# Kernel tuning notes

Hardware: AMD Instinct MI355X
Metric: run time of the kernel (lower is better)

Reference implementation:

```python
import math
import jax, jax.numpy as jnp
import numpy as np

# config (matches env defaults of the torch module, scaled to production size)
V, D, L, NH, NKV, MLP_M, RECUR, N_VB = 32768, 1024, 6, 16, 8, 3, 2, 5
BG_BK, BG_DIM = 4096, 128
HD = D // NH            # 64 head dim
KV = NKV * HD           # 512 kv width
B, T = 2, 1024
SOFTCAP = 30.0
EPS = 1.1920929e-07     # fp32 eps used by F.rms_norm(eps=None)


def _rms(x):
    return x * jax.lax.rsqrt(jnp.mean(jnp.square(x), axis=-1, keepdims=True) + EPS)


def _rope(x, c, s):
    h = x.shape[-1] // 2
    x1, x2 = x[..., :h], x[..., h:]
    return jnp.concatenate([x1 * c + x2 * s, -x1 * s + x2 * c], axis=-1)


def _forward(ids, tgt, emb, bg_embed, bg_proj, bg_scale, ve,
             Wq, Wk, Wv, Wo, qg, a_s, m_s, mix, Wfc, Wpr):
    Bz, Tz = ids.shape
    # token embedding + bigram-hash embedding
    x = emb[ids]
    t = ids.astype(jnp.int32)
    hv = jnp.bitwise_xor(t[:, 1:] * 36313, t[:, :-1] * 27191) % (BG_BK - 1)
    h = jnp.zeros_like(t).at[:, 1:].set(hv)
    bg = (bg_embed[h] @ bg_proj) * bg_scale
    x = _rms(x + bg)
    x0 = x
    # rope tables
    inv = 1.0 / (10000.0 ** (jnp.arange(0, HD, 2, dtype=jnp.float32) / HD))
    ang = jnp.arange(Tz, dtype=jnp.float32)[:, None] * inv      # (T, HD/2)
    c, s = jnp.cos(ang)[None, None], jnp.sin(ang)[None, None]   # (1,1,T,HD/2)
    mask = jnp.tril(jnp.ones((Tz, Tz), dtype=bool))
    eff = 0
    for _ in range(RECUR):
        for l in range(L):
            vel = ve[eff % N_VB][ids]                            # (B,T,KV)
            m = mix[l]
            x = m[0] * x + m[1] * x0
            # attention
            xn = _rms(x)
            q = (xn @ Wq[l]).reshape(Bz, Tz, NH, HD).transpose(0, 2, 1, 3)
            k = (xn @ Wk[l]).reshape(Bz, Tz, NKV, HD).transpose(0, 2, 1, 3)
            v = ((xn @ Wv[l]) + vel).reshape(Bz, Tz, NKV, HD).transpose(0, 2, 1, 3)
            q, k = _rms(q), _rms(k)
            q, k = _rope(q, c, s), _rope(k, c, s)
            q = q * qg[l][None, :, None, None]
            rep = NH // NKV                                      # GQA expand
            kf = jnp.repeat(k, rep, axis=1)
            vf = jnp.repeat(v, rep, axis=1)
            sc = jnp.einsum('bhqd,bhkd->bhqk', q, kf) / math.sqrt(HD)
            sc = jnp.where(mask, sc, -jnp.inf)
            att = jax.nn.softmax(sc, axis=-1)
            y = jnp.einsum('bhqk,bhkd->bhqd', att, vf)
            y = y.transpose(0, 2, 1, 3).reshape(Bz, Tz, D) @ Wo[l]
            x = x + a_s[l] * y
            # mlp: relu(fc(x))^2 @ proj
            hmid = jnp.square(jax.nn.relu(_rms(x) @ Wfc[l]))
            x = x + m_s[l] * (hmid @ Wpr[l])
            eff += 1
    x = _rms(x)
    lo = x @ emb.T
    lo = SOFTCAP * jnp.tanh(lo / SOFTCAP)
    logp = jax.nn.log_softmax(lo, axis=-1)
    nll = -jnp.take_along_axis(logp, tgt[..., None], axis=-1)[..., 0]
    return jnp.mean(nll)


def setup_inputs() -> dict:
    key = jax.random.key(0)
    ks = jax.random.split(key, 14)
    def nrm(k, shape, std):
        return std * jax.random.normal(k, shape, dtype=jnp.float32)
    eff = L * RECUR
    return {
        'ids': jax.random.randint(ks[0], (B, T), 0, V),
        'tgt': jax.random.randint(ks[1], (B, T), 0, V),
        'emb': nrm(ks[2], (V, D), 0.005),
        'bg_embed': nrm(ks[3], (BG_BK, BG_DIM), 0.02),
        'bg_proj': nrm(ks[4], (BG_DIM, D), 1.0 / math.sqrt(BG_DIM)),
        'bg_scale': jnp.float32(0.05),
        've': nrm(ks[5], (N_VB, V, KV), 0.01),
        'Wq': nrm(ks[6], (L, D, D), 1.0 / math.sqrt(D)),
        'Wk': nrm(ks[7], (L, D, KV), 1.0 / math.sqrt(D)),
        'Wv': nrm(ks[8], (L, D, KV), 1.0 / math.sqrt(D)),
        'Wo': nrm(ks[9], (L, D, D), 1.0 / (math.sqrt(D) * math.sqrt(2 * eff))),
        'qg': jnp.full((L, NH), 1.5, jnp.float32),
        'a_s': jnp.ones((L, D), jnp.float32),
        'm_s': jnp.ones((L, D), jnp.float32),
        'mix': jnp.stack([jnp.ones((L, D)), jnp.zeros((L, D))], axis=1).astype(jnp.float32),
        'Wfc': nrm(ks[10], (L, D, MLP_M * D), 1.0 / math.sqrt(D)),
        'Wpr': nrm(ks[11], (L, MLP_M * D, D), 1.0 / (math.sqrt(MLP_M * D) * math.sqrt(2 * eff))),
    }


def reference(ids, tgt, emb, bg_embed, bg_proj, bg_scale, ve,
              Wq, Wk, Wv, Wo, qg, a_s, m_s, mix, Wfc, Wpr):
    return _forward(ids, tgt, emb, bg_embed, bg_proj, bg_scale, ve,
                    Wq, Wk, Wv, Wo, qg, a_s, m_s, mix, Wfc, Wpr)
```

## Files before the change

### kernel.cpp

```cpp
#include <hip/hip_runtime.h>
#include <hip/hip_bf16.h>
#include <math.h>

#define DEV __device__ __forceinline__

typedef unsigned short u16;
typedef short bf16x8 __attribute__((ext_vector_type(8)));
typedef float f32x4 __attribute__((ext_vector_type(4)));
typedef u16 u16x8 __attribute__((ext_vector_type(8)));
typedef u16 u16x4 __attribute__((ext_vector_type(4)));

#define T_SEQ 1024
#define NTOK 2048
#define DIM 1024
#define NHD 16
#define NKVH 8
#define HDIM 64
#define KVD 512
#define MLPD 3072
#define VOC 32768
#define EPSF 1.1920929e-07f
#define SCAP 30.0f
#define NCB 512

#define MEMFENCE asm volatile("" ::: "memory")

DEV u16 f2b(float f) {
  __hip_bfloat16 h = __float2bfloat16(f);
  u16 r; __builtin_memcpy(&r, &h, 2); return r;
}
DEV float b2f(u16 u) {
  __hip_bfloat16 h; __builtin_memcpy(&h, &u, 2);
  return __bfloat162float(h);
}

DEV void gload16(const void* g, void* l) {
  __builtin_amdgcn_global_load_lds((const __attribute__((address_space(1))) void*)g,
                                   (__attribute__((address_space(3))) void*)l, 16, 0, 0);
}

DEV float blk_sum256(float v, float* sbuf) {
#pragma unroll
  for (int o = 32; o; o >>= 1) v += __shfl_xor(v, o, 64);
  int w = threadIdx.x >> 6;
  if ((threadIdx.x & 63) == 0) sbuf[w] = v;
  __syncthreads();
  return sbuf[0] + sbuf[1] + sbuf[2] + sbuf[3];
}

__global__ __launch_bounds__(256) void transpose_f2b(const float* __restrict__ in,
    u16* __restrict__ out, int K, int N, size_t in_ls, size_t out_ls) {
  __shared__ float tile[32][33];
  int l = blockIdx.z;
  const float* src = in + (size_t)l * in_ls;
  u16* dst = out + (size_t)l * out_ls;
  int k0 = blockIdx.y << 5, n0 = blockIdx.x << 5;
  int tx = threadIdx.x & 31, ty = threadIdx.x >> 5;
#pragma unroll
  for (int i = 0; i < 32; i += 8)
    tile[ty + i][tx] = src[(size_t)(k0 + ty + i) * N + n0 + tx];
  __syncthreads();
#pragma unroll
  for (int i = 0; i < 32; i += 8)
    dst[(size_t)(n0 + ty + i) * K + k0 + tx] = f2b(tile[tx][ty + i]);
}

__global__ __launch_bounds__(256) void f2b_copy(const float* __restrict__ in,
    u16* __restrict__ out, size_t n) {
  size_t i = ((size_t)blockIdx.x * 256 + threadIdx.x) * 8;
  if (i >= n) return;
  float4 a = *(const float4*)(in + i);
  float4 b = *(const float4*)(in + i + 4);
  u16x8 o;
  o[0] = f2b(a.x); o[1] = f2b(a.y); o[2] = f2b(a.z); o[3] = f2b(a.w);
  o[4] = f2b(b.x); o[5] = f2b(b.y); o[6] = f2b(b.z); o[7] = f2b(b.w);
  *(u16x8*)(out + i) = o;
}

__global__ __launch_bounds__(256) void rope_table(float* __restrict__ rc, float* __restrict__ rs) {
  int idx = blockIdx.x * 256 + threadIdx.x;
  if (idx >= T_SEQ * 32) return;
  int t = idx >> 5, i = idx & 31;
  float inv = expf(-((float)(2 * i) / (float)HDIM) * logf(10000.0f));
  float ang = (float)t * inv;
  rc[idx] = cosf(ang);
  rs[idx] = sinf(ang);
}

__global__ __launch_bounds__(256) void embed_kernel(const int* __restrict__ ids,
    const float* __restrict__ emb, const float* __restrict__ bg_embed,
    const float* __restrict__ bg_proj, const float* __restrict__ bg_scale_p,
    float* __restrict__ x, float* __restrict__ x0) {
  __shared__ float be[128];
  __shared__ float sbuf[4];
  int tok = blockIdx.x, tid = threadIdx.x;
  int t = tok & (T_SEQ - 1);
  int id = ids[tok];
  int hsh = 0;
  if (t > 0) {
    int prev = ids[tok - 1];
    hsh = ((id * 36313) ^ (prev * 27191)) % 4095;
  }
  if (tid < 128) be[tid] = bg_embed[hsh * 128 + tid];
  __syncthreads();
  float scale = bg_scale_p[0];
  const float4* bp = (const float4*)bg_proj;
  float ax = 0.f, ay = 0.f, az = 0.f, aw = 0.f;
#pragma unroll 4
  for (int j = 0; j < 128; ++j) {
    float bj = be[j];
    float4 p = bp[j * 256 + tid];
    ax += bj * p.x; ay += bj * p.y; az += bj * p.z; aw += bj * p.w;
  }
  float4 e = *(const float4*)(emb + (size_t)id * DIM + tid * 4);
  float vx = e.x + ax * scale, vy = e.y + ay * scale;
  float vz = e.z + az * scale, vw = e.w + aw * scale;
  float ss = vx * vx + vy * vy + vz * vz + vw * vw;
  float tot = blk_sum256(ss, sbuf);
  float rn = rsqrtf(tot * (1.0f / DIM) + EPSF);
  float4 o; o.x = vx * rn; o.y = vy * rn; o.z = vz * rn; o.w = vw * rn;
  size_t base = (size_t)tok * DIM + tid * 4;
  *(float4*)(x + base) = o;
  *(float4*)(x0 + base) = o;
}

__global__ __launch_bounds__(256) void mix_rms(float* __restrict__ x,
    const float* __restrict__ x0, const float* __restrict__ mixl, u16* __restrict__ xn) {
  __shared__ float sbuf[4];
  int tok = blockIdx.x, tid = threadIdx.x;
  size_t base = (size_t)tok * DIM + tid * 4;
  float4 a = *(const float4*)(x + base);
  float4 b = *(const float4*)(x0 + base);
  float4 m0 = *(const float4*)(mixl + tid * 4);
  float4 m1 = *(const float4*)(mixl + DIM + tid * 4);
  float rx = m0.x * a.x + m1.x * b.x;
  float ry = m0.y * a.y + m1.y * b.y;
  float rz = m0.z * a.z + m1.z * b.z;
  float rw = m0.w * a.w + m1.w * b.w;
  float ss = rx * rx + ry * ry + rz * rz + rw * rw;
  float tot = blk_sum256(ss, sbuf);
  float rn = rsqrtf(tot * (1.0f / DIM) + EPSF);
  float4 o; o.x = rx; o.y = ry; o.z = rz; o.w = rw;
  *(float4*)(x + base) = o;
  u16x4 q;
  q[0] = f2b(rx * rn); q[1] = f2b(ry * rn); q[2] = f2b(rz * rn); q[3] = f2b(rw * rn);
  *(u16x4*)(xn + base) = q;
}

__global__ __launch_bounds__(256) void rms_only(const float* __restrict__ x, u16* __restrict__ out) {
  __shared__ float sbuf[4];
  int tok = blockIdx.x, tid = threadIdx.x;
  size_t base = (size_t)tok * DIM + tid * 4;
  float4 a = *(const float4*)(x + base);
  float ss = a.x * a.x + a.y * a.y + a.z * a.z + a.w * a.w;
  float tot = blk_sum256(ss, sbuf);
  float rn = rsqrtf(tot * (1.0f / DIM) + EPSF);
  u16x4 q;
  q[0] = f2b(a.x * rn); q[1] = f2b(a.y * rn); q[2] = f2b(a.z * rn); q[3] = f2b(a.w * rn);
  *(u16x4*)(out + base) = q;
}

template <int EPI, int BN>
__global__ __launch_bounds__(256, (BN == 64 ? 3 : 2)) void gemm_bt(
    const u16* __restrict__ A, const u16* __restrict__ Bt,
    float* __restrict__ Cf, u16* __restrict__ Cb, const float* __restrict__ colscale,
    int N, int K, int kpn) {
  constexpr int MF = (BN == 128) ? 4 : 2;
  constexpr int ASZ = 128 * 64;
  constexpr int BSZ = BN * 64;
  constexpr int NLD = 4 + BN / 32;
  __shared__ u16 As[2 * ASZ];
  __shared__ u16 Bs[2 * BSZ];
  int tid = threadIdx.x;
  int wid = tid >> 6, lane = tid & 63;
  int g = lane >> 4, c = lane & 15;
  int row0 = blockIdx.y << 7, col0 = blockIdx.x * BN;
  int kbase = blockIdx.z * kpn;
  int wr = (BN == 128) ? ((wid >> 1) << 6) : (wid << 5);
  int wc = (BN == 128) ? ((wid & 1) << 6) : 0;
  f32x4 acc[MF][4] = {};

  int sr = lane >> 3;
  int kb = lane & 7;
  const u16* srcA[4];
  int ldsA[4];
#pragma unroll
  for (int i = 0; i < 4; ++i) {
    int s = (wid << 2) + i;
    int r = (s << 3) + sr;
    srcA[i] = A + (size_t)(row0 + r) * K + kbase + ((kb ^ (r & 7)) << 3);
    ldsA[i] = s << 9;
  }
  const u16* srcB[BN / 32];
  int ldsB[BN / 32];
#pragma unroll
  for (int i = 0; i < BN / 32; ++i) {
    int s = wid * (BN / 32) + i;
    int r = (s << 3) + sr;
    srcB[i] = Bt + (size_t)(col0 + r) * K + kbase + ((kb ^ (r & 7)) << 3);
    ldsB[i] = s << 9;
  }

#pragma unroll
  for (int i = 0; i < 4; ++i) gload16(srcA[i], As + ldsA[i]);
#pragma unroll
  for (int i = 0; i < BN / 32; ++i) gload16(srcB[i], Bs + ldsB[i]);

  int nk = kpn >> 6;
  for (int t = 0; t < nk; ++t) {
    int cur = t & 1;
    if (t + 1 < nk) {
      int nxt = cur ^ 1;
      int ko = (t + 1) << 6;
#pragma unroll
      for (int i = 0; i < 4; ++i) gload16(srcA[i] + ko, As + nxt * ASZ + ldsA[i]);
#pragma unroll
      for (int i = 0; i < BN / 32; ++i) gload16(srcB[i] + ko, Bs + nxt * BSZ + ldsB[i]);
      if constexpr (NLD == 6) asm volatile("s_waitcnt vmcnt(6)" ::: "memory");
      else asm volatile("s_waitcnt vmcnt(8)" ::: "memory");
    } else {
      asm volatile("s_waitcnt vmcnt(0)" ::: "memory");
    }
    __builtin_amdgcn_s_barrier();
    MEMFENCE;
    const u16* ab = As + cur * ASZ;
    const u16* bb = Bs + cur * BSZ;
#pragma unroll
    for (int ks = 0; ks < 2; ++ks) {
      bf16x8 af[MF], bfr[4];
#pragma unroll
      for (int m = 0; m < MF; ++m) {
        int r = wr + m * 16 + c;
        int kbs = ((ks << 2) + g) ^ (r & 7);
        af[m] = *(const bf16x8*)(ab + r * 64 + (kbs << 3));
      }
#pragma unroll
      for (int n = 0; n < 4; ++n) {
        int r = wc + n * 16 + c;
        int kbs = ((ks << 2) + g) ^ (r & 7);
        bfr[n] = *(const bf16x8*)(bb + r * 64 + (kbs << 3));
      }
      __builtin_amdgcn_s_setprio(1);
#pragma unroll
      for (int m = 0; m < MF; ++m)
#pragma unroll
        for (int n = 0; n < 4; ++n)
          acc[m][n] = __builtin_amdgcn_mfma_f32_16x16x32_bf16(af[m], bfr[n], acc[m][n], 0, 0, 0);
      __builtin_amdgcn_s_setprio(0);
    }
    MEMFENCE;
    __builtin_amdgcn_s_barrier();
  }

#pragma unroll
  for (int m = 0; m < MF; ++m) {
#pragma unroll
    for (int n = 0; n < 4; ++n) {
      int gcol = col0 + wc + n * 16 + c;
#pragma unroll
      for (int j = 0; j < 4; ++j) {
        int grow = row0 + wr + m * 16 + g * 4 + j;
        float v = acc[m][n][j];
        if (EPI == 1) {
          atomicAdd(&Cf[(size_t)grow * N + gcol], colscale[gcol] * v);
        } else if (EPI == 2) {
          float r = v > 0.f ? v : 0.f;
          Cb[(size_t)grow * N + gcol] = f2b(r * r);
        }
      }
    }
  }
}

__global__ __launch_bounds__(512, 2) void gemm_lmhead(
    const u16* __restrict__ A, const u16* __restrict__ Bt,
    const int* __restrict__ tgt, float* __restrict__ pM, float* __restrict__ pS,
    float* __restrict__ loTgt) {
  constexpr int K = 1024;
  constexpr int TSZ = 256 * 64;
  __shared__ u16 As[2 * TSZ];
  __shared__ u16 Bs[2 * TSZ];
  int tid = threadIdx.x;
  int wid = tid >> 6, lane = tid & 63;
  int wm = wid >> 2, wn = wid & 3;
  int g = lane >> 4, c = lane & 15;
  int row0 = blockIdx.y << 8, col0 = blockIdx.x << 8;
  f32x4 acc[8][4] = {};

  int sr = lane >> 3, kb = lane & 7;
  const u16* srcA[4];
  const u16* srcB[4];
  int ldsOff[4];
#pragma unroll
  for (int i = 0; i < 4; ++i) {
    int s = (wid << 2) + i;
    int r = (s << 3) + sr;
    srcA[i] = A + (size_t)(row0 + r) * K + ((kb ^ (r & 7)) << 3);
    srcB[i] = Bt + (size_t)(col0 + r) * K + ((kb ^ (r & 7)) << 3);
    ldsOff[i] = s << 9;
  }

#pragma unroll
  for (int i = 0; i < 4; ++i) {
    gload16(srcA[i], As + ldsOff[i]);
    gload16(srcB[i], Bs + ldsOff[i]);
  }

  constexpr int nk = K >> 6;
  for (int kt = 0; kt < nk; ++kt) {
    int cur = kt & 1;
    if (kt + 1 < nk) {
      int nxt = cur ^ 1;
      int ko = (kt + 1) << 6;
#pragma unroll
      for (int i = 0; i < 4; ++i) {
        gload16(srcA[i] + ko, As + nxt * TSZ + ldsOff[i]);
        gload16(srcB[i] + ko, Bs + nxt * TSZ + ldsOff[i]);
      }
      asm volatile("s_waitcnt vmcnt(8)" ::: "memory");
    } else {
      asm volatile("s_waitcnt vmcnt(0)" ::: "memory");
    }
    __builtin_amdgcn_s_barrier();
    MEMFENCE;
    const u16* ab = As + cur * TSZ;
    const u16* bb = Bs + cur * TSZ;
    bf16x8 bfr[4][2];
#pragma unroll
    for (int nf = 0; nf < 4; ++nf) {
      int r = (wn << 6) + nf * 16 + c;
#pragma unroll
      for (int ks = 0; ks < 2; ++ks) {
        int kbs = ((ks << 2) + g) ^ (r & 7);
        bfr[nf][ks] = *(const bf16x8*)(bb + r * 64 + (kbs << 3));
      }
    }
#pragma unroll
    for (int p = 0; p < 4; ++p) {
      bf16x8 af[2][2];
#pragma unroll
      for (int mi = 0; mi < 2; ++mi) {
        int r = (wm << 7) + ((p << 1) + mi) * 16 + c;
#pragma unroll
        for (int ks = 0; ks < 2; ++ks) {
          int kbs = ((ks << 2) + g) ^ (r & 7);
          af[mi][ks] = *(const bf16x8*)(ab + r * 64 + (kbs << 3));
        }
      }
      __builtin_amdgcn_s_setprio(1);
#pragma unroll
      for (int ks = 0; ks < 2; ++ks)
#pragma unroll
        for (int mi = 0; mi < 2; ++mi)
#pragma unroll
          for (int nf = 0; nf < 4; ++nf)
            acc[(p << 1) + mi][nf] = __builtin_amdgcn_mfma_f32_16x16x32_bf16(
                af[mi][ks], bfr[nf][ks], acc[(p << 1) + mi][nf], 0, 0, 0);
      __builtin_amdgcn_s_setprio(0);
    }
    MEMFENCE;
    __builtin_amdgcn_s_barrier();
  }

  int cb = (col0 >> 6) + wn;
#pragma unroll
  for (int mf = 0; mf < 8; ++mf) {
#pragma unroll
    for (int j = 0; j < 4; ++j) {
      int grow = row0 + (wm << 7) + mf * 16 + g * 4 + j;
      int tg = tgt[grow];
      float sv[4];
      float mx = -3.0e38f;
#pragma unroll
      for (int nf = 0; nf < 4; ++nf) {
        float a = acc[mf][nf][j] * (1.0f / SCAP);
        a = fminf(fmaxf(a, -15.f), 15.f);
        float e = __expf(2.0f * a);
        float tt = SCAP * (e - 1.0f) / (e + 1.0f);
        sv[nf] = tt;
        mx = fmaxf(mx, tt);
        int gcol = col0 + (wn << 6) + nf * 16 + c;
        if (gcol == tg) loTgt[grow] = tt;
      }
      mx = fmaxf(mx, __shfl_xor(mx, 1, 64));
      mx = fmaxf(mx, __shfl_xor(mx, 2, 64));
      mx = fmaxf(mx, __shfl_xor(mx, 4, 64));
      mx = fmaxf(mx, __shfl_xor(mx, 8, 64));
      float s = 0.f;
#pragma unroll
      for (int nf = 0; nf < 4; ++nf) s += __expf(sv[nf] - mx);
      s += __shfl_xor(s, 1, 64);
      s += __shfl_xor(s, 2, 64);
      s += __shfl_xor(s, 4, 64);
      s += __shfl_xor(s, 8, 64);
      if (c == 0) {
        pM[(size_t)grow * NCB + cb] = mx;
        pS[(size_t)grow * NCB + cb] = s;
      }
    }
  }
}

__global__ __launch_bounds__(256, 3) void gemm_qkv(
    const u16* __restrict__ A, const u16* __restrict__ Bt,
    const float* __restrict__ qg_l, const float* __restrict__ rc, const float* __restrict__ rs,
    const float* __restrict__ ve, const int* __restrict__ ids, int vb,
    u16* __restrict__ qB, u16* __restrict__ kB, u16* __restrict__ vT) {
  constexpr int K = 1024;
  constexpr int ASZ = 128 * 64;
  constexpr int BSZ = 64 * 64;
  __shared__ u16 As[2 * ASZ];
  __shared__ u16 Bs[2 * BSZ];
  int tid = threadIdx.x;
  int wid = tid >> 6, lane = tid & 63;
  int g = lane >> 4, c = lane & 15;
  int bx = blockIdx.x;
  int row0 = blockIdx.y << 7, col0 = bx << 6;
  f32x4 acc[2][4] = {};

  int sr = lane >> 3, kb = lane & 7;
  const u16* srcA[4];
  int ldsA[4];
#pragma unroll
  for (int i = 0; i < 4; ++i) {
    int s = (wid << 2) + i;
    int r = (s << 3) + sr;
    srcA[i] = A + (size_t)(row0 + r) * K + ((kb ^ (r & 7)) << 3);
    ldsA[i] = s << 9;
  }
  const u16* srcB[2];
  int ldsB[2];
#pragma unroll
  for (int i = 0; i < 2; ++i) {
    int s = (wid << 1) + i;
    int r = (s << 3) + sr;
    srcB[i] = Bt + (size_t)(col0 + r) * K + ((kb ^ (r & 7)) << 3);
    ldsB[i] = s << 9;
  }

#pragma unroll
  for (int i = 0; i < 4; ++i) gload16(srcA[i], As + ldsA[i]);
#pragma unroll
  for (int i = 0; i < 2; ++i) gload16(srcB[i], Bs + ldsB[i]);

  for (int t = 0; t < 16; ++t) {
    int cur = t & 1;
    if (t + 1 < 16) {
      int nxt = cur ^ 1;
      int ko = (t + 1) << 6;
#pragma unroll
      for (int i = 0; i < 4; ++i) gload16(srcA[i] + ko, As + nxt * ASZ + ldsA[i]);
#pragma unroll
      for (int i = 0; i < 2; ++i) gload16(srcB[i] + ko, Bs + nxt * BSZ + ldsB[i]);
      asm volatile("s_waitcnt vmcnt(6)" ::: "memory");
    } else {
      asm volatile("s_waitcnt vmcnt(0)" ::: "memory");
    }
    __builtin_amdgcn_s_barrier();
    MEMFENCE;
    const u16* ab = As + cur * ASZ;
    const u16* bb = Bs + cur * BSZ;
#pragma unroll
    for (int ks = 0; ks < 2; ++ks) {
      bf16x8 af[2], bfr[4];
#pragma unroll
      for (int m = 0; m < 2; ++m) {
        int r = (wid << 5) + m * 16 + c;
        int kbs = ((ks << 2) + g) ^ (r & 7);
        af[m] = *(const bf16x8*)(ab + r * 64 + (kbs << 3));
      }
#pragma unroll
      for (int n = 0; n < 4; ++n) {
        int r = n * 16 + c;
        int kbs = ((ks << 2) + g) ^ (r & 7);
        bfr[n] = *(const bf16x8*)(bb + r * 64 + (kbs << 3));
      }
      __builtin_amdgcn_s_setprio(1);
#pragma unroll
      for (int m = 0; m < 2; ++m)
#pragma unroll
        for (int n = 0; n < 4; ++n)
          acc[m][n] = __builtin_amdgcn_mfma_f32_16x16x32_bf16(af[m], bfr[n], acc[m][n], 0, 0, 0);
      __builtin_amdgcn_s_setprio(0);
    }
    MEMFENCE;
    __builtin_amdgcn_s_barrier();
  }

  int b = row0 >> 10;
  if (bx < 24) {
    bool isq = (bx < 16);
    int h = isq ? bx : bx - 16;
    float gmul = isq ? qg_l[h] * 0.125f : 1.0f;
    u16* hb = isq ? (qB + ((size_t)(b * NHD + h)) * T_SEQ * HDIM)
                  : (kB + ((size_t)(b * NKVH + h)) * T_SEQ * HDIM);
#pragma unroll
    for (int m = 0; m < 2; ++m) {
#pragma unroll
      for (int j = 0; j < 4; ++j) {
        int grow = row0 + (wid << 5) + m * 16 + g * 4 + j;
        int t = grow & (T_SEQ - 1);
        float vv[4];
        float ss = 0.f;
#pragma unroll
        for (int n = 0; n < 4; ++n) { vv[n] = acc[m][n][j]; ss += vv[n] * vv[n]; }
        ss += __shfl_xor(ss, 1, 64);
        ss += __shfl_xor(ss, 2, 64);
        ss += __shfl_xor(ss, 4, 64);
        ss += __shfl_xor(ss, 8, 64);
        float rn = rsqrtf(ss * (1.0f / HDIM) + EPSF);
#pragma unroll
        for (int n = 0; n < 4; ++n) vv[n] *= rn;
        float c0 = rc[t * 32 + c], s0 = rs[t * 32 + c];
        float c1 = rc[t * 32 + 16 + c], s1 = rs[t * 32 + 16 + c];
        float o0 = vv[0] * c0 + vv[2] * s0;
        float o1 = vv[1] * c1 + vv[3] * s1;
        float o2 = vv[2] * c0 - vv[0] * s0;
        float o3 = vv[3] * c1 - vv[1] * s1;
        u16* dst = hb + (size_t)t * HDIM;
        dst[c] = f2b(o0 * gmul);
        dst[16 + c] = f2b(o1 * gmul);
        dst[32 + c] = f2b(o2 * gmul);
        dst[48 + c] = f2b(o3 * gmul);
      }
    }
  } else {
    int kh = bx - 24;
#pragma unroll
    for (int m = 0; m < 2; ++m) {
#pragma unroll
      for (int j = 0; j < 4; ++j) {
        int grow = row0 + (wid << 5) + m * 16 + g * 4 + j;
        int lr = (wid << 5) + m * 16 + g * 4 + j;
        int id = ids[grow];
        const float* vl = ve + ((size_t)vb * VOC + id) * KVD + kh * HDIM;
#pragma unroll
        for (int n = 0; n < 4; ++n)
          As[lr * 72 + n * 16 + c] = f2b(acc[m][n][j] + vl[n * 16 + c]);
      }
    }
    __syncthreads();
    int hd = tid & 63, seg = tid >> 6;
    int t0 = (row0 & (T_SEQ - 1)) + seg * 32;
    u16* dst = vT + (((size_t)(b * NKVH + kh)) * HDIM + hd) * T_SEQ + t0;
#pragma unroll
    for (int i = 0; i < 32; i += 8) {
      u16x8 o;
#pragma unroll
      for (int e = 0; e < 8; ++e) o[e] = As[(seg * 32 + i + e) * 72 + hd];
      *(u16x8*)(dst + i) = o;
    }
  }
}

__global__ __launch_bounds__(128) void attn_kernel(const u16* __restrict__ qB,
    const u16* __restrict__ kB, const u16* __restrict__ vT, const float* __restrict__ qg_l,
    u16* __restrict__ attout) {
  __shared__ u16 plds[2][32 * 76];
  int b = blockIdx.z, h = blockIdx.y;
  int kh = h >> 1;
  int wid = threadIdx.x >> 6, lane = threadIdx.x & 63;
  int g = lane >> 4, c = lane & 15;
  int strip = wid ? (31 - (int)blockIdx.x) : (int)blockIdx.x;
  int qr0 = strip << 5;
  const u16* qptr = qB + ((size_t)(b * NHD + h)) * T_SEQ * HDIM;
  const u16* kptr = kB + ((size_t)(b * NKVH + kh)) * T_SEQ * HDIM;
  const u16* vptr = vT + ((size_t)(b * NKVH + kh)) * HDIM * T_SEQ;
  u16* pw = plds[wid];
  float Mh = fabsf(qg_l[h]) * 8.0f;

  bf16x8 aq[2][2];
#pragma unroll
  for (int m = 0; m < 2; ++m)
#pragma unroll
    for (int ks = 0; ks < 2; ++ks)
      aq[m][ks] = *(const bf16x8*)(qptr + (qr0 + m * 16 + c) * HDIM + ks * 32 + g * 8);

  bf16x8 vone;
#pragma unroll
  for (int e = 0; e < 8; ++e) vone[e] = (short)0x3F80;

  f32x4 oacc[2][4] = {};
  f32x4 lacc[2] = {};

  for (int kv0 = 0; kv0 <= qr0; kv0 += 64) {
    bf16x8 bk[4][2];
#pragma unroll
    for (int n = 0; n < 4; ++n)
#pragma unroll
      for (int ks = 0; ks < 2; ++ks)
        bk[n][ks] = *(const bf16x8*)(kptr + (kv0 + n * 16 + c) * HDIM + ks * 32 + g * 8);
    f32x4 sc[2][4] = {};
#pragma unroll
    for (int ks = 0; ks < 2; ++ks)
#pragma unroll
      for (int m = 0; m < 2; ++m)
#pragma unroll
        for (int n = 0; n < 4; ++n)
          sc[m][n] = __builtin_amdgcn_mfma_f32_16x16x32_bf16(aq[m][ks], bk[n][ks], sc[m][n], 0, 0, 0);
    bool maskT = (kv0 + 64 > qr0);
#pragma unroll
    for (int m = 0; m < 2; ++m) {
#pragma unroll
      for (int j = 0; j < 4; ++j) {
        int row = qr0 + m * 16 + g * 4 + j;
        float p0 = __expf(sc[m][0][j] - Mh);
        float p1 = __expf(sc[m][1][j] - Mh);
        float p2 = __expf(sc[m][2][j] - Mh);
        float p3 = __expf(sc[m][3][j] - Mh);
        if (maskT) {
          if (kv0 + c > row) p0 = 0.f;
          if (kv0 + 16 + c > row) p1 = 0.f;
          if (kv0 + 32 + c > row) p2 = 0.f;
          if (kv0 + 48 + c > row) p3 = 0.f;
        }
        int pr = m * 16 + g * 4 + j;
        pw[pr * 76 + c] = f2b(p0);
        pw[pr * 76 + 16 + c] = f2b(p1);
        pw[pr * 76 + 32 + c] = f2b(p2);
        pw[pr * 76 + 48 + c] = f2b(p3);
      }
    }
    MEMFENCE;
    bf16x8 ap[2][2];
#pragma unroll
    for (int m = 0; m < 2; ++m)
#pragma unroll
      for (int ks = 0; ks < 2; ++ks) {
        u16x8 tmp = *(const u16x8*)(pw + (m * 16 + c) * 76 + ks * 32 + g * 8);
        __builtin_memcpy(&ap[m][ks], &tmp, 16);
      }
    bf16x8 bv[4][2];
#pragma unroll
    for (int n = 0; n < 4; ++n)
#pragma unroll
      for (int ks = 0; ks < 2; ++ks)
        bv[n][ks] = *(const bf16x8*)(vptr + (n * 16 + c) * T_SEQ + kv0 + ks * 32 + g * 8);
#pragma unroll
    for (int ks = 0; ks < 2; ++ks) {
#pragma unroll
      for (int m = 0; m < 2; ++m) {
#pragma unroll
        for (int n = 0; n < 4; ++n)
          oacc[m][n] = __builtin_amdgcn_mfma_f32_16x16x32_bf16(ap[m][ks], bv[n][ks], oacc[m][n], 0, 0, 0);
        lacc[m] = __builtin_amdgcn_mfma_f32_16x16x32_bf16(ap[m][ks], vone, lacc[m], 0, 0, 0);
      }
    }
  }

#pragma unroll
  for (int m = 0; m < 2; ++m) {
#pragma unroll
    for (int j = 0; j < 4; ++j) {
      float inv = 1.0f / lacc[m][j];
      int trow = qr0 + m * 16 + g * 4 + j;
      u16* orow = attout + ((size_t)(b * T_SEQ + trow)) * DIM + h * HDIM;
#pragma unroll
      for (int n = 0; n < 4; ++n)
        orow[n * 16 + c] = f2b(oacc[m][n][j] * inv);
    }
  }
}

__global__ __launch_bounds__(256) void lse_merge(const float* __restrict__ pM,
    const float* __restrict__ pS, const float* __restrict__ loTgt, float* __restrict__ nll) {
  __shared__ float sbuf[4];
  int tok = blockIdx.x, tid = threadIdx.x;
  int wid = tid >> 6, lane = tid & 63;
  const float* rm = pM + (size_t)tok * NCB;
  const float* rs = pS + (size_t)tok * NCB;
  float m0 = rm[tid], m1 = rm[tid + 256];
  float mx = fmaxf(m0, m1);
#pragma unroll
  for (int o = 32; o; o >>= 1) mx = fmaxf(mx, __shfl_xor(mx, o, 64));
  if (lane == 0) sbuf[wid] = mx;
  __syncthreads();
  float M = fmaxf(fmaxf(sbuf[0], sbuf[1]), fmaxf(sbuf[2], sbuf[3]));
  __syncthreads();
  float s = rs[tid] * __expf(m0 - M) + rs[tid + 256] * __expf(m1 - M);
  float S = blk_sum256(s, sbuf);
  if (tid == 0) nll[tok] = logf(S) + M - loTgt[tok];
}

__global__ __launch_bounds__(256) void loss_final(const float* __restrict__ nll,
    float* __restrict__ out) {
  __shared__ float sbuf[4];
  int tid = threadIdx.x;
  float acc = 0.f;
  for (int i = tid; i < NTOK; i += 256) acc += nll[i];
  float tot = blk_sum256(acc, sbuf);
  if (tid == 0) out[0] = tot * (1.0f / NTOK);
}

extern "C" void kernel_launch(void* const* d_in, const int* in_sizes, int n_in,
                              void* d_out, int out_size, void* d_ws, size_t ws_size,
                              hipStream_t stream) {
  (void)in_sizes; (void)n_in; (void)out_size; (void)ws_size;
  const int* ids = (const int*)d_in[0];
  const int* tgt = (const int*)d_in[1];
  const float* emb = (const float*)d_in[2];
  const float* bg_embed = (const float*)d_in[3];
  const float* bg_proj = (const float*)d_in[4];
  const float* bg_scale = (const float*)d_in[5];
  const float* ve = (const float*)d_in[6];
  const float* Wq = (const float*)d_in[7];
  const float* Wk = (const float*)d_in[8];
  const float* Wv = (const float*)d_in[9];
  const float* Wo = (const float*)d_in[10];
  const float* qg = (const float*)d_in[11];
  const float* a_s = (const float*)d_in[12];
  const float* m_s = (const float*)d_in[13];
  const float* mix = (const float*)d_in[14];
  const float* Wfc = (const float*)d_in[15];
  const float* Wpr = (const float*)d_in[16];

  char* w = (char*)d_ws;
  auto alloc = [&](size_t bytes) {
    char* p = w;
    w += (bytes + 255) & ~(size_t)255;
    return p;
  };
  u16* WqkvT = (u16*)alloc(6ull * 2048 * 1024 * 2);
  u16* WoT   = (u16*)alloc(6ull * 1024 * 1024 * 2);
  u16* WfcT  = (u16*)alloc(6ull * 3072 * 1024 * 2);
  u16* WprT  = (u16*)alloc(6ull * 1024 * 3072 * 2);
  u16* embB  = (u16*)alloc((size_t)VOC * DIM * 2);
  float* x   = (float*)alloc((size_t)NTOK * DIM * 4);
  float* x0  = (float*)alloc((size_t)NTOK * DIM * 4);
  u16* xn    = (u16*)alloc((size_t)NTOK * DIM * 2);
  u16* qBuf  = (u16*)alloc((size_t)NTOK * DIM * 2);
  u16* kBuf  = (u16*)alloc((size_t)NTOK * KVD * 2);
  u16* vTb   = (u16*)alloc((size_t)NTOK * KVD * 2);
  u16* attout = (u16*)alloc((size_t)NTOK * DIM * 2);
  u16* xmlp  = (u16*)alloc((size_t)NTOK * DIM * 2);
  u16* hmid  = (u16*)alloc((size_t)NTOK * MLPD * 2);
  float* rc  = (float*)alloc((size_t)T_SEQ * 32 * 4);
  float* rs  = (float*)alloc((size_t)T_SEQ * 32 * 4);
  float* pM  = (float*)alloc((size_t)NTOK * NCB * 4);
  float* pS  = (float*)alloc((size_t)NTOK * NCB * 4);
  float* loTgt = (float*)alloc(NTOK * 4);
  float* nll = (float*)alloc(NTOK * 4);

  transpose_f2b<<<dim3(32, 32, 6), 256, 0, stream>>>(Wq, WqkvT, 1024, 1024,
      (size_t)1024 * 1024, (size_t)2048 * 1024);
  transpose_f2b<<<dim3(16, 32, 6), 256, 0, stream>>>(Wk, WqkvT + 1024 * 1024, 1024, 512,
      (size_t)1024 * 512, (size_t)2048 * 1024);
  transpose_f2b<<<dim3(16, 32, 6), 256, 0, stream>>>(Wv, WqkvT + 1536 * 1024, 1024, 512,
      (size_t)1024 * 512, (size_t)2048 * 1024);
  transpose_f2b<<<dim3(32, 32, 6), 256, 0, stream>>>(Wo, WoT, 1024, 1024,
      (size_t)1024 * 1024, (size_t)1024 * 1024);
  transpose_f2b<<<dim3(96, 32, 6), 256, 0, stream>>>(Wfc, WfcT, 1024, 3072,
      (size_t)1024 * 3072, (size_t)3072 * 1024);
  transpose_f2b<<<dim3(32, 96, 6), 256, 0, stream>>>(Wpr, WprT, 3072, 1024,
      (size_t)3072 * 1024, (size_t)1024 * 3072);
  f2b_copy<<<16384, 256, 0, stream>>>(emb, embB, (size_t)VOC * DIM);
  rope_table<<<128, 256, 0, stream>>>(rc, rs);
  embed_kernel<<<NTOK, 256, 0, stream>>>(ids, emb, bg_embed, bg_proj, bg_scale, x, x0);

  for (int step = 0; step < 12; ++step) {
    int l = step % 6;
    mix_rms<<<NTOK, 256, 0, stream>>>(x, x0, mix + l * 2048, xn);
    gemm_qkv<<<dim3(32, 16), 256, 0, stream>>>(xn, WqkvT + (size_t)l * 2048 * 1024,
        qg + l * 16, rc, rs, ve, ids, step % 5, qBuf, kBuf, vTb);
    attn_kernel<<<dim3(16, 16, 2), 128, 0, stream>>>(qBuf, kBuf, vTb, qg + l * 16, attout);
    gemm_bt<1, 64><<<dim3(16, 16, 2), 256, 0, stream>>>(attout, WoT + (size_t)l * 1024 * 1024,
        x, nullptr, a_s + l * DIM, 1024, 1024, 512);
    rms_only<<<NTOK, 256, 0, stream>>>(x, xmlp);
    gemm_bt<2, 128><<<dim3(24, 16, 1), 256, 0, stream>>>(xmlp, WfcT + (size_t)l * 3072 * 1024,
        nullptr, hmid, nullptr, 3072, 1024, 1024);
    gemm_bt<1, 64><<<dim3(16, 16, 3), 256, 0, stream>>>(hmid, WprT + (size_t)l * 1024 * 3072,
        x, nullptr, m_s + l * DIM, 1024, 3072, 1024);
  }

  rms_only<<<NTOK, 256, 0, stream>>>(x, xn);
  gemm_lmhead<<<dim3(128, 8), 512, 0, stream>>>(xn, embB, tgt, pM, pS, loTgt);
  lse_merge<<<NTOK, 256, 0, stream>>>(pM, pS, loTgt, nll);
  loss_final<<<1, 256, 0, stream>>>(nll, (float*)d_out);
}
```

Baseline: 2.089 ms.

## Replace split-K atomic accumulation with partial buffers reduced in norm kernels

The split-K output-projection and MLP-projection GEMMs now write plain stores into per-split partial buffers instead of doing float atomicAdd into the residual. The following norm kernel sums the partials, applies the per-column scale, updates the residual and computes the RMS norm, which merges mix_rms and rms_only into one templated kernel. The LM-head GEMM also gets a 1D grid with a block-index swizzle so blocks sharing the same weight columns run close together, for better L2 reuse. The cost is a 24MB partial buffer and more memory traffic in the norm kernels.

```diff
diff --git a/kernel.cpp b/kernel.cpp
--- a/kernel.cpp
+++ b/kernel.cpp
@@ -22,6 +22,7 @@
 #define EPSF 1.1920929e-07f
 #define SCAP 30.0f
 #define NCB 512
+#define PSTRIDE ((size_t)NTOK * DIM)
 
 #define MEMFENCE asm volatile("" ::: "memory")
 
@@ -124,46 +125,50 @@
   *(float4*)(x0 + base) = o;
 }
 
-__global__ __launch_bounds__(256) void mix_rms(float* __restrict__ x,
-    const float* __restrict__ x0, const float* __restrict__ mixl, u16* __restrict__ xn) {
+template <int NP, int MIX>
+__global__ __launch_bounds__(256) void norm_k(float* __restrict__ x,
+    const float* __restrict__ parts, const float* __restrict__ colscale,
+    const float* __restrict__ mixl, const float* __restrict__ x0,
+    u16* __restrict__ xn) {
   __shared__ float sbuf[4];
   int tok = blockIdx.x, tid = threadIdx.x;
   size_t base = (size_t)tok * DIM + tid * 4;
   float4 a = *(const float4*)(x + base);
-  float4 b = *(const float4*)(x0 + base);
-  float4 m0 = *(const float4*)(mixl + tid * 4);
-  float4 m1 = *(const float4*)(mixl + DIM + tid * 4);
-  float rx = m0.x * a.x + m1.x * b.x;
-  float ry = m0.y * a.y + m1.y * b.y;
-  float rz = m0.z * a.z + m1.z * b.z;
-  float rw = m0.w * a.w + m1.w * b.w;
-  float ss = rx * rx + ry * ry + rz * rz + rw * rw;
-  float tot = blk_sum256(ss, sbuf);
-  float rn = rsqrtf(tot * (1.0f / DIM) + EPSF);
-  float4 o; o.x = rx; o.y = ry; o.z = rz; o.w = rw;
-  *(float4*)(x + base) = o;
-  u16x4 q;
-  q[0] = f2b(rx * rn); q[1] = f2b(ry * rn); q[2] = f2b(rz * rn); q[3] = f2b(rw * rn);
-  *(u16x4*)(xn + base) = q;
-}
-
-__global__ __launch_bounds__(256) void rms_only(const float* __restrict__ x, u16* __restrict__ out) {
-  __shared__ float sbuf[4];
-  int tok = blockIdx.x, tid = threadIdx.x;
-  size_t base = (size_t)tok * DIM + tid * 4;
-  float4 a = *(const float4*)(x + base);
+  if (NP > 0) {
+    float4 cs = *(const float4*)(colscale + tid * 4);
+    float4 s = *(const float4*)(parts + base);
+    {
+      float4 p = *(const float4*)(parts + PSTRIDE + base);
+      s.x += p.x; s.y += p.y; s.z += p.z; s.w += p.w;
+    }
+    if (NP == 3) {
+      float4 p = *(const float4*)(parts + 2 * PSTRIDE + base);
+      s.x += p.x; s.y += p.y; s.z += p.z; s.w += p.w;
+    }
+    a.x += cs.x * s.x; a.y += cs.y * s.y; a.z += cs.z * s.z; a.w += cs.w * s.w;
+  }
+  if (MIX) {
+    float4 m0 = *(const float4*)(mixl + tid * 4);
+    float4 m1 = *(const float4*)(mixl + DIM + tid * 4);
+    float4 b = *(const float4*)(x0 + base);
+    a.x = m0.x * a.x + m1.x * b.x;
+    a.y = m0.y * a.y + m1.y * b.y;
+    a.z = m0.z * a.z + m1.z * b.z;
+    a.w = m0.w * a.w + m1.w * b.w;
+  }
   float ss = a.x * a.x + a.y * a.y + a.z * a.z + a.w * a.w;
   float tot = blk_sum256(ss, sbuf);
   float rn = rsqrtf(tot * (1.0f / DIM) + EPSF);
+  if (NP > 0 || MIX) *(float4*)(x + base) = a;
   u16x4 q;
   q[0] = f2b(a.x * rn); q[1] = f2b(a.y * rn); q[2] = f2b(a.z * rn); q[3] = f2b(a.w * rn);
-  *(u16x4*)(out + base) = q;
+  *(u16x4*)(xn + base) = q;
 }
 
 template <int EPI, int BN>
 __global__ __launch_bounds__(256, (BN == 64 ? 3 : 2)) void gemm_bt(
     const u16* __restrict__ A, const u16* __restrict__ Bt,
-    float* __restrict__ Cf, u16* __restrict__ Cb, const float* __restrict__ colscale,
+    float* __restrict__ Cf, u16* __restrict__ Cb,
     int N, int K, int kpn) {
   constexpr int MF = (BN == 128) ? 4 : 2;
   constexpr int ASZ = 128 * 64;
@@ -252,6 +257,7 @@
     __builtin_amdgcn_s_barrier();
   }
 
+  size_t zoff = (size_t)blockIdx.z * PSTRIDE;
 #pragma unroll
   for (int m = 0; m < MF; ++m) {
 #pragma unroll
@@ -262,7 +268,7 @@
         int grow = row0 + wr + m * 16 + g * 4 + j;
         float v = acc[m][n][j];
         if (EPI == 1) {
-          atomicAdd(&Cf[(size_t)grow * N + gcol], colscale[gcol] * v);
+          Cf[zoff + (size_t)grow * N + gcol] = v;
         } else if (EPI == 2) {
           float r = v > 0.f ? v : 0.f;
           Cb[(size_t)grow * N + gcol] = f2b(r * r);
@@ -284,7 +290,10 @@
   int wid = tid >> 6, lane = tid & 63;
   int wm = wid >> 2, wn = wid & 3;
   int g = lane >> 4, c = lane & 15;
-  int row0 = blockIdx.y << 8, col0 = blockIdx.x << 8;
+  int bid = blockIdx.x;
+  int swz = ((bid & 7) << 7) + (bid >> 3);
+  int colb = swz >> 3, rowb = swz & 7;
+  int row0 = rowb << 8, col0 = colb << 8;
   f32x4 acc[8][4] = {};
 
   int sr = lane >> 3, kb = lane & 7;
@@ -379,7 +388,7 @@
         float tt = SCAP * (e - 1.0f) / (e + 1.0f);
         sv[nf] = tt;
         mx = fmaxf(mx, tt);
-        int gcol = col0 + (wn << 6) + nf * 16 + c;
+        int gcol = (colb << 8) + (wn << 6) + nf * 16 + c;
         if (gcol == tg) loTgt[grow] = tt;
       }
       mx = fmaxf(mx, __shfl_xor(mx, 1, 64));
@@ -734,6 +743,7 @@
   u16* attout = (u16*)alloc((size_t)NTOK * DIM * 2);
   u16* xmlp  = (u16*)alloc((size_t)NTOK * DIM * 2);
   u16* hmid  = (u16*)alloc((size_t)NTOK * MLPD * 2);
+  float* pparts = (float*)alloc(3 * PSTRIDE * 4);
   float* rc  = (float*)alloc((size_t)T_SEQ * 32 * 4);
   float* rs  = (float*)alloc((size_t)T_SEQ * 32 * 4);
   float* pM  = (float*)alloc((size_t)NTOK * NCB * 4);
@@ -757,23 +767,28 @@
   rope_table<<<128, 256, 0, stream>>>(rc, rs);
   embed_kernel<<<NTOK, 256, 0, stream>>>(ids, emb, bg_embed, bg_proj, bg_scale, x, x0);
 
+  int lprev = 0;
   for (int step = 0; step < 12; ++step) {
     int l = step % 6;
-    mix_rms<<<NTOK, 256, 0, stream>>>(x, x0, mix + l * 2048, xn);
+    if (step == 0)
+      norm_k<0, 1><<<NTOK, 256, 0, stream>>>(x, nullptr, nullptr, mix + l * 2048, x0, xn);
+    else
+      norm_k<3, 1><<<NTOK, 256, 0, stream>>>(x, pparts, m_s + lprev * DIM, mix + l * 2048, x0, xn);
     gemm_qkv<<<dim3(32, 16), 256, 0, stream>>>(xn, WqkvT + (size_t)l * 2048 * 1024,
         qg + l * 16, rc, rs, ve, ids, step % 5, qBuf, kBuf, vTb);
     attn_kernel<<<dim3(16, 16, 2), 128, 0, stream>>>(qBuf, kBuf, vTb, qg + l * 16, attout);
     gemm_bt<1, 64><<<dim3(16, 16, 2), 256, 0, stream>>>(attout, WoT + (size_t)l * 1024 * 1024,
-        x, nullptr, a_s + l * DIM, 1024, 1024, 512);
-    rms_only<<<NTOK, 256, 0, stream>>>(x, xmlp);
+        pparts, nullptr, 1024, 1024, 512);
+    norm_k<2, 0><<<NTOK, 256, 0, stream>>>(x, pparts, a_s + l * DIM, nullptr, nullptr, xmlp);
     gemm_bt<2, 128><<<dim3(24, 16, 1), 256, 0, stream>>>(xmlp, WfcT + (size_t)l * 3072 * 1024,
-        nullptr, hmid, nullptr, 3072, 1024, 1024);
+        nullptr, hmid, 3072, 1024, 1024);
     gemm_bt<1, 64><<<dim3(16, 16, 3), 256, 0, stream>>>(hmid, WprT + (size_t)l * 1024 * 3072,
-        x, nullptr, m_s + l * DIM, 1024, 3072, 1024);
-  }
-
-  rms_only<<<NTOK, 256, 0, stream>>>(x, xn);
-  gemm_lmhead<<<dim3(128, 8), 512, 0, stream>>>(xn, embB, tgt, pM, pS, loTgt);
+        pparts, nullptr, 1024, 3072, 1024);
+    lprev = l;
+  }
+
+  norm_k<3, 0><<<NTOK, 256, 0, stream>>>(x, pparts, m_s + lprev * DIM, nullptr, nullptr, xn);
+  gemm_lmhead<<<1024, 512, 0, stream>>>(xn, embB, tgt, pM, pS, loTgt);
   lse_merge<<<NTOK, 256, 0, stream>>>(pM, pS, loTgt, nll);
   loss_final<<<1, 256, 0, stream>>>(nll, (float*)d_out);
 }
```

Result: faster. 1.939 ms (-7.2%).
